# Kernel optimization log

Measured on AMD Instinct MI355X. Metric: run time of the kernel, lower is better.

Reference implementation:

```python
import jax, jax.numpy as jnp
import numpy as np

B, C, T = 128, 19, 1000

def _conv2d(x, w, pad, groups=1):
    return jax.lax.conv_general_dilated(x, w, (1, 1), [(pad[0], pad[0]), (pad[1], pad[1])],
                                        dimension_numbers=('NCHW', 'OIHW', 'NCHW'),
                                        feature_group_count=groups)

def _conv1d(x, w, pad):
    return jax.lax.conv_general_dilated(x, w, (1,), [(pad, pad)],
                                        dimension_numbers=('NCH', 'OIH', 'NCH'))

def _bn(x, g, b, axis=1):
    # eval-mode BatchNorm with running_mean=0, running_var=1 -> pure affine
    shp = [1] * x.ndim
    shp[axis] = -1
    return x * g.reshape(shp) + b.reshape(shp)

def _gat(x, W, a_src, a_dst, bias, src, dst, ew):
    # GATConv, concat=False (head mean); messages scaled by external edge weight ew
    N = x.shape[0]
    H, D = a_src.shape
    h = (x @ W).reshape(N, H, D)
    e = jax.nn.leaky_relu((h * a_src).sum(-1)[src] + (h * a_dst).sum(-1)[dst], 0.2)  # [E,H]
    emax = jax.ops.segment_max(e, dst, num_segments=N)
    ee = jnp.exp(e - emax[dst])
    alpha = ee / (jax.ops.segment_sum(ee, dst, num_segments=N)[dst] + 1e-16)
    msg = (alpha * ew[:, None])[:, :, None] * h[src]  # [E,H,D]
    return jax.ops.segment_sum(msg, dst, num_segments=N).mean(1) + bias

def setup_inputs():
    key = jax.random.key(0)
    ks = iter(jax.random.split(key, 48))
    def nrm(shape, s=0.1):
        return jax.random.normal(next(ks), shape, jnp.float32) * s
    ii = np.arange(C)
    base = np.arange(B)[:, None] * C
    src = (base + np.repeat(ii, C)[None, :]).reshape(-1)
    dst = (base + np.tile(ii, C)[None, :]).reshape(-1)
    return {
        'x': nrm((B, C, T), 1.0),
        'conv1_w': nrm((16, 1, 1, 25)),
        'bn1_g': 1.0 + nrm((16,)), 'bn1_b': nrm((16,)),
        'depth_w': nrm((16, 1, C, 1)),
        'bn2_g': 1.0 + nrm((16,)), 'bn2_b': nrm((16,)),
        'se_w1': nrm((16, 4)), 'se_w2': nrm((4, 16)),
        'sep_w': nrm((16, 16, 1, 16)),
        'bn3_g': 1.0 + nrm((16,)), 'bn3_b': nrm((16,)),
        'ms_w0': nrm((16, 1, 15)), 'ms_g0': 1.0 + nrm((16,)), 'ms_b0': nrm((16,)),
        'ms_w1': nrm((16, 1, 25)), 'ms_g1': 1.0 + nrm((16,)), 'ms_b1': nrm((16,)),
        'ms_w2': nrm((16, 1, 35)), 'ms_g2': 1.0 + nrm((16,)), 'ms_b2': nrm((16,)),
        'adj_w': nrm((32, 1)), 'adj_b': nrm((1,)),
        'gat1_w': nrm((32, 8 * 64), 0.05), 'gat1_as': nrm((8, 64)), 'gat1_ad': nrm((8, 64)), 'gat1_bias': nrm((64,)),
        'skip1_w': nrm((32, 64)), 'skip1_b': nrm((64,)),
        'bng1_g': 1.0 + nrm((64,)), 'bng1_b': nrm((64,)),
        'gat2_w': nrm((64, 8 * 64), 0.05), 'gat2_as': nrm((8, 64)), 'gat2_ad': nrm((8, 64)), 'gat2_bias': nrm((64,)),
        'bng2_g': 1.0 + nrm((64,)), 'bng2_b': nrm((64,)),
        'cls_w1': nrm((64, 64)), 'cls_b1': nrm((64,)),
        'cls_w2': nrm((64, 2)), 'cls_b2': nrm((2,)),
        'edge_index': jnp.asarray(np.stack([src, dst]), dtype=jnp.int32),
        'batch_idx': jnp.repeat(jnp.arange(B, dtype=jnp.int32), C),
    }

def reference(x, conv1_w, bn1_g, bn1_b, depth_w, bn2_g, bn2_b, se_w1, se_w2, sep_w, bn3_g, bn3_b,
              ms_w0, ms_g0, ms_b0, ms_w1, ms_g1, ms_b1, ms_w2, ms_g2, ms_b2,
              adj_w, adj_b, gat1_w, gat1_as, gat1_ad, gat1_bias, skip1_w, skip1_b, bng1_g, bng1_b,
              gat2_w, gat2_as, gat2_ad, gat2_bias, bng2_g, bng2_b, cls_w1, cls_b1, cls_w2, cls_b2,
              edge_index, batch_idx):
    Bn, Cn, Tn = x.shape
    gelu = lambda v: jax.nn.gelu(v, approximate=False)
    # --- EEGNet-style frontend ---
    y = _conv2d(x[:, None], conv1_w, (0, 12))                 # [B,16,C,T]
    y = _bn(y, bn1_g, bn1_b)
    y = _conv2d(y, depth_w, (0, 0), groups=16)                # depthwise over channels -> [B,16,1,T]
    y = jax.nn.elu(_bn(y, bn2_g, bn2_b))
    s = y.mean((2, 3))                                        # SE squeeze [B,16]
    s = jax.nn.sigmoid(gelu(s @ se_w1) @ se_w2)
    y = y * s[:, :, None, None]
    y = y.reshape(Bn, 16, 1, Tn // 4, 4).mean(-1)             # AvgPool2d((1,4))
    y = jax.nn.elu(_bn(_conv2d(y, sep_w, (0, 8)), bn3_g, bn3_b))
    yv = y.mean((2, 3))                                       # AdaptiveAvgPool2d((C,1)): 1->C replicates
    y_nodes = jnp.broadcast_to(yv[:, None, :], (Bn, Cn, 16)).reshape(Bn * Cn, 16)
    # --- per-channel multiscale conv1d ---
    z = x.reshape(Bn * Cn, 1, Tn)
    acc = jax.nn.elu(_bn(_conv1d(z, ms_w0, 7), ms_g0, ms_b0))
    acc = acc + jax.nn.elu(_bn(_conv1d(z, ms_w1, 12), ms_g1, ms_b1))
    acc = acc + jax.nn.elu(_bn(_conv1d(z, ms_w2, 17), ms_g2, ms_b2))
    z = (acc / 3.0).mean(-1)                                  # AdaptiveAvgPool1d(1) -> [N,16]
    feat = jnp.concatenate([y_nodes, z], axis=1)              # [N,32]
    # --- edge-weighted GAT stack ---
    scores = jax.nn.sigmoid(feat @ adj_w + adj_b).reshape(-1)
    src, dst = edge_index[0], edge_index[1]
    ew = scores[src] * scores[dst]
    h = _gat(feat, gat1_w, gat1_as, gat1_ad, gat1_bias, src, dst, ew)
    h = gelu(_bn(h, bng1_g, bng1_b) + feat @ skip1_w + skip1_b)
    h2 = _gat(h, gat2_w, gat2_as, gat2_ad, gat2_bias, src, dst, ew)
    h = gelu(_bn(h2, bng2_g, bng2_b) + h2)
    # --- global mean pool + classifier ---
    gs = jax.ops.segment_sum(h, batch_idx, num_segments=Bn)
    cnt = jax.ops.segment_sum(jnp.ones((Bn * Cn, 1), h.dtype), batch_idx, num_segments=Bn)
    g = gs / cnt
    return gelu(g @ cls_w1 + cls_b1) @ cls_w2 + cls_b2
```

## Files before the change

kernel.cpp:

```cpp
#include <hip/hip_runtime.h>
#include <hip/hip_bf16.h>
#include <math.h>

#define BATCH 128
#define NCH 19
#define TLEN 1000
#define NNODES (BATCH * NCH)

__device__ __forceinline__ float eluf(float x) {
  return fmaxf(x, 0.f) + (__expf(fminf(x, 0.f)) - 1.f);
}
__device__ __forceinline__ float geluf(float x) { return 0.5f * x * (1.f + erff(x * 0.70710678118654752f)); }
__device__ __forceinline__ float sigf(float x) { return 1.f / (1.f + __expf(-x)); }
__device__ __forceinline__ float lrelu(float x) { return x > 0.f ? x : 0.2f * x; }

__global__ __launch_bounds__(256) void k_pool(
    const float* __restrict__ x, const float* __restrict__ w1,
    const float* __restrict__ bn1g, const float* __restrict__ bn1b,
    const float* __restrict__ dw, const float* __restrict__ bn2g,
    const float* __restrict__ bn2b, float* __restrict__ y4g,
    float* __restrict__ ssum) {
  int blk = blockIdx.x;
  int b = blk >> 4, f = blk & 15;
  int tid = threadIdx.x;
  __shared__ float xw[1024];
  __shared__ float dws[19], w1s[25];
  __shared__ float redw[4];
  if (tid < 19) dws[tid] = dw[f * 19 + tid];
  else if (tid >= 32 && tid < 57) w1s[tid - 32] = w1[f * 25 + tid - 32];
  __syncthreads();
  const float* xb = x + (size_t)b * NCH * TLEN;
  for (int i = tid; i < 1024; i += 256) {
    int t = i - 12;
    float v = 0.f;
    if (t >= 0 && t < TLEN) {
#pragma unroll
      for (int c = 0; c < 19; c++) v += dws[c] * xb[c * TLEN + t];
    }
    xw[i] = v;
  }
  __syncthreads();
  float g1 = bn1g[f], b1 = bn1b[f];
  float g2 = bn2g[f], b2 = bn2b[f];
  float sumdw = 0.f;
#pragma unroll
  for (int c = 0; c < 19; c++) sumdw += dws[c];
  float scale = g2 * g1, cb = g2 * b1 * sumdw + b2;
  float part = 0.f;
  if (tid < 250) {
    float pool = 0.f;
#pragma unroll
    for (int q = 0; q < 4; q++) {
      int t = 4 * tid + q;
      float acc = 0.f;
#pragma unroll
      for (int k = 0; k < 25; k++) acc += w1s[k] * xw[t + k];
      pool += eluf(scale * acc + cb);
    }
    part = pool;
    y4g[(size_t)(b * 16 + f) * 250 + tid] = pool * 0.25f;
  }
  int lane = tid & 63, wid = tid >> 6;
  for (int off = 32; off > 0; off >>= 1) part += __shfl_down(part, off, 64);
  if (lane == 0) redw[wid] = part;
  __syncthreads();
  if (tid == 0) ssum[b * 16 + f] = redw[0] + redw[1] + redw[2] + redw[3];
}

__global__ __launch_bounds__(256) void k_sep(
    const float* __restrict__ y4g, const float* __restrict__ ssum,
    const float* __restrict__ sew1, const float* __restrict__ sew2,
    const float* __restrict__ sw, const float* __restrict__ g3,
    const float* __restrict__ b3, float* __restrict__ yv) {
  int blk = blockIdx.x;
  int b = blk >> 4, fo = blk & 15;
  int tid = threadIdx.x;
  __shared__ float yloc[16 * 268];
  __shared__ float sws[256];
  __shared__ float s_s[16], se_s[16], u4[4];
  __shared__ float redw[4];
  sws[tid] = sw[fo * 256 + tid];
  if (tid < 16) s_s[tid] = ssum[b * 16 + tid] * (1.f / 1000.f);
  __syncthreads();
  if (tid < 4) {
    float a = 0.f;
#pragma unroll
    for (int ff = 0; ff < 16; ff++) a += s_s[ff] * sew1[ff * 4 + tid];
    u4[tid] = geluf(a);
  }
  __syncthreads();
  if (tid < 16) {
    float a = 0.f;
#pragma unroll
    for (int j = 0; j < 4; j++) a += u4[j] * sew2[j * 16 + tid];
    se_s[tid] = sigf(a);
  }
  __syncthreads();
#pragma unroll
  for (int fi = 0; fi < 16; fi++) {
    float sc = se_s[fi];
    const float* yr = y4g + (size_t)(b * 16 + fi) * 250;
    for (int j = tid; j < 268; j += 256) {
      float v = (j >= 8 && j < 258) ? yr[j - 8] * sc : 0.f;
      yloc[fi * 268 + j] = v;
    }
  }
  __syncthreads();
  float accsum = 0.f;
  if (tid < 251) {
    float acc = 0.f;
#pragma unroll
    for (int fi = 0; fi < 16; fi++) {
      const float* yr = &yloc[fi * 268 + tid];
      const float* wp = &sws[fi * 16];
#pragma unroll
      for (int k = 0; k < 16; k++) acc += yr[k] * wp[k];
    }
    accsum = eluf(g3[fo] * acc + b3[fo]);
  }
  int lane = tid & 63, wid = tid >> 6;
  for (int off = 32; off > 0; off >>= 1)
    accsum += __shfl_down(accsum, off, 64);
  if (lane == 0) redw[wid] = accsum;
  __syncthreads();
  if (tid == 0)
    yv[b * 16 + fo] = (redw[0] + redw[1] + redw[2] + redw[3]) * (1.f / 251.f);
}

#define RP 8
__global__ __launch_bounds__(256) void k_ms(
    const float* __restrict__ x, const float* __restrict__ w0,
    const float* __restrict__ ga0, const float* __restrict__ bb0,
    const float* __restrict__ w1, const float* __restrict__ ga1,
    const float* __restrict__ bb1, const float* __restrict__ w2,
    const float* __restrict__ ga2, const float* __restrict__ bb2,
    const float* __restrict__ yv, float* __restrict__ feat) {
  int n = blockIdx.x, tid = threadIdx.x;
  __shared__ float xr[1034];
  __shared__ float wst[1200];
  __shared__ float red[256];
  for (int i = tid; i < 1034; i += 256) {
    int t = i - 17;
    xr[i] = (t >= 0 && t < TLEN) ? x[(size_t)n * TLEN + t] : 0.f;
  }
  for (int i = tid; i < 240; i += 256) wst[i] = w0[i];
  for (int i = tid; i < 400; i += 256) wst[240 + i] = w1[i];
  for (int i = tid; i < 560; i += 256) wst[640 + i] = w2[i];
  __syncthreads();

  int f = tid & 15, plane = tid >> 4;
  float z = 0.f;

  {
    float w[15];
#pragma unroll
    for (int k = 0; k < 15; k++) w[k] = wst[f * 15 + k];
    float g = ga0[f], c = bb0[f];
    for (int base = plane * RP; base < TLEN; base += 16 * RP) {
      float xv[14 + RP];
#pragma unroll
      for (int i = 0; i < 14 + RP; i++) xv[i] = xr[base + 10 + i];
#pragma unroll
      for (int r = 0; r < RP; r++) {
        float a = 0.f;
#pragma unroll
        for (int k = 0; k < 15; k++) a += xv[r + k] * w[k];
        z += eluf(g * a + c);
      }
    }
  }
  {
    float w[25];
#pragma unroll
    for (int k = 0; k < 25; k++) w[k] = wst[240 + f * 25 + k];
    float g = ga1[f], c = bb1[f];
    for (int base = plane * RP; base < TLEN; base += 16 * RP) {
      float xv[24 + RP];
#pragma unroll
      for (int i = 0; i < 24 + RP; i++) xv[i] = xr[base + 5 + i];
#pragma unroll
      for (int r = 0; r < RP; r++) {
        float a = 0.f;
#pragma unroll
        for (int k = 0; k < 25; k++) a += xv[r + k] * w[k];
        z += eluf(g * a + c);
      }
    }
  }
  {
    float w[35];
#pragma unroll
    for (int k = 0; k < 35; k++) w[k] = wst[640 + f * 35 + k];
    float g = ga2[f], c = bb2[f];
    for (int base = plane * RP; base < TLEN; base += 16 * RP) {
      float xv[34 + RP];
#pragma unroll
      for (int i = 0; i < 34 + RP; i++) xv[i] = xr[base + i];
#pragma unroll
      for (int r = 0; r < RP; r++) {
        float a = 0.f;
#pragma unroll
        for (int k = 0; k < 35; k++) a += xv[r + k] * w[k];
        z += eluf(g * a + c);
      }
    }
  }

  red[tid] = z;
  __syncthreads();
  for (int s = 128; s >= 16; s >>= 1) {
    if (tid < s) red[tid] += red[tid + s];
    __syncthreads();
  }
  if (tid < 16) {
    feat[(size_t)n * 32 + 16 + tid] = red[tid] * (1.f / 3000.f);
    feat[(size_t)n * 32 + tid] = yv[(n / 19) * 16 + tid];
  }
}

__global__ __launch_bounds__(256) void k_gat1(
    const float* __restrict__ feat, const float* __restrict__ adjw,
    const float* __restrict__ adjb, const float* __restrict__ gw,
    const float* __restrict__ gas, const float* __restrict__ gad,
    const float* __restrict__ gbias, const float* __restrict__ skw,
    const float* __restrict__ skb, const float* __restrict__ bg,
    const float* __restrict__ bb, float* __restrict__ sc_out,
    float* __restrict__ hfeat) {
  int b = blockIdx.x, tid = threadIdx.x;
  __shared__ float fb[19 * 32];
  __shared__ float h1[19 * 512];
  __shared__ float as_s[19 * 8], ad_s[19 * 8], sc_s[19];
  __shared__ float watt[19 * 8 * 19];
  for (int i = tid; i < 19 * 32; i += 256) fb[i] = feat[(size_t)b * 19 * 32 + i];
  __syncthreads();
  for (int idx = tid; idx < 19 * 512; idx += 256) {
    int i = idx >> 9, o = idx & 511;
    const float* fr = &fb[i * 32];
    float a = 0.f;
#pragma unroll
    for (int c = 0; c < 32; c++) a += fr[c] * gw[c * 512 + o];
    h1[idx] = a;
  }
  if (tid < 19) {
    float a = adjb[0];
#pragma unroll
    for (int c = 0; c < 32; c++) a += fb[tid * 32 + c] * adjw[c];
    float s = sigf(a);
    sc_s[tid] = s;
    sc_out[b * 19 + tid] = s;
  }
  __syncthreads();
  if (tid < 152) {
    int i = tid / 8, h = tid & 7;
    float a = 0.f, d2 = 0.f;
#pragma unroll
    for (int d = 0; d < 64; d++) {
      float hv = h1[i * 512 + h * 64 + d];
      a += hv * gas[h * 64 + d];
      d2 += hv * gad[h * 64 + d];
    }
    as_s[tid] = a;
    ad_s[tid] = d2;
  }
  __syncthreads();
  if (tid < 152) {
    int j = tid / 8, h = tid & 7;
    float adj_ = ad_s[j * 8 + h];
    float ev[19], m = -1e30f;
#pragma unroll
    for (int i = 0; i < 19; i++) {
      float e = lrelu(as_s[i * 8 + h] + adj_);
      ev[i] = e;
      m = fmaxf(m, e);
    }
    float den = 0.f;
#pragma unroll
    for (int i = 0; i < 19; i++) {
      ev[i] = __expf(ev[i] - m);
      den += ev[i];
    }
    float inv = 1.f / (den + 1e-16f);
    float scj = sc_s[j];
#pragma unroll
    for (int i = 0; i < 19; i++)
      watt[(j * 8 + h) * 19 + i] = ev[i] * inv * sc_s[i] * scj;
  }
  __syncthreads();
  for (int idx = tid; idx < 19 * 64; idx += 256) {
    int j = idx >> 6, d = idx & 63;
    float acc = 0.f;
#pragma unroll
    for (int h = 0; h < 8; h++) {
      const float* wr = &watt[(j * 8 + h) * 19];
      float a = 0.f;
#pragma unroll
      for (int i = 0; i < 19; i++) a += wr[i] * h1[i * 512 + h * 64 + d];
      acc += a;
    }
    float om = acc * 0.125f + gbias[d];
    float v = bg[d] * om + bb[d];
    float sk = skb[d];
    const float* fr = &fb[j * 32];
#pragma unroll
    for (int c = 0; c < 32; c++) sk += fr[c] * skw[c * 64 + d];
    hfeat[(size_t)(b * 19 + j) * 64 + d] = geluf(v + sk);
  }
}

__global__ __launch_bounds__(256) void k_gat2(
    const float* __restrict__ hfeat, const float* __restrict__ sc_ws,
    const float* __restrict__ gw, const float* __restrict__ gas,
    const float* __restrict__ gad, const float* __restrict__ gbias,
    const float* __restrict__ bg, const float* __restrict__ bb,
    const float* __restrict__ cw1, const float* __restrict__ cb1,
    const float* __restrict__ cw2, const float* __restrict__ cb2,
    float* __restrict__ out) {
  int b = blockIdx.x, tid = threadIdx.x;
  __shared__ float hb[19 * 64];
  __shared__ float h2[19 * 512];
  __shared__ float as_s[19 * 8], ad_s[19 * 8], sc_s[19];
  __shared__ float watt[19 * 8 * 19];
  __shared__ float hout[19 * 64];
  __shared__ float gpool[64], u_s[64];
  for (int i = tid; i < 19 * 64; i += 256) hb[i] = hfeat[(size_t)b * 19 * 64 + i];
  if (tid < 19) sc_s[tid] = sc_ws[b * 19 + tid];
  __syncthreads();
  for (int idx = tid; idx < 19 * 512; idx += 256) {
    int i = idx >> 9, o = idx & 511;
    const float* hr = &hb[i * 64];
    float a = 0.f;
#pragma unroll
    for (int c = 0; c < 64; c++) a += hr[c] * gw[c * 512 + o];
    h2[idx] = a;
  }
  __syncthreads();
  if (tid < 152) {
    int i = tid / 8, h = tid & 7;
    float a = 0.f, d2 = 0.f;
#pragma unroll
    for (int d = 0; d < 64; d++) {
      float hv = h2[i * 512 + h * 64 + d];
      a += hv * gas[h * 64 + d];
      d2 += hv * gad[h * 64 + d];
    }
    as_s[tid] = a;
    ad_s[tid] = d2;
  }
  __syncthreads();
  if (tid < 152) {
    int j = tid / 8, h = tid & 7;
    float adj_ = ad_s[j * 8 + h];
    float ev[19], m = -1e30f;
#pragma unroll
    for (int i = 0; i < 19; i++) {
      float e = lrelu(as_s[i * 8 + h] + adj_);
      ev[i] = e;
      m = fmaxf(m, e);
    }
    float den = 0.f;
#pragma unroll
    for (int i = 0; i < 19; i++) {
      ev[i] = __expf(ev[i] - m);
      den += ev[i];
    }
    float inv = 1.f / (den + 1e-16f);
    float scj = sc_s[j];
#pragma unroll
    for (int i = 0; i < 19; i++)
      watt[(j * 8 + h) * 19 + i] = ev[i] * inv * sc_s[i] * scj;
  }
  __syncthreads();
  for (int idx = tid; idx < 19 * 64; idx += 256) {
    int j = idx >> 6, d = idx & 63;
    float acc = 0.f;
#pragma unroll
    for (int h = 0; h < 8; h++) {
      const float* wr = &watt[(j * 8 + h) * 19];
      float a = 0.f;
#pragma unroll
      for (int i = 0; i < 19; i++) a += wr[i] * h2[i * 512 + h * 64 + d];
      acc += a;
    }
    float om = acc * 0.125f + gbias[d];
    float v = bg[d] * om + bb[d] + om;
    hout[idx] = geluf(v);
  }
  __syncthreads();
  if (tid < 64) {
    float a = 0.f;
#pragma unroll
    for (int j = 0; j < 19; j++) a += hout[j * 64 + tid];
    gpool[tid] = a * (1.f / 19.f);
  }
  __syncthreads();
  if (tid < 64) {
    float a = cb1[tid];
#pragma unroll
    for (int d = 0; d < 64; d++) a += gpool[d] * cw1[d * 64 + tid];
    u_s[tid] = geluf(a);
  }
  __syncthreads();
  if (tid < 2) {
    float a = cb2[tid];
#pragma unroll
    for (int e = 0; e < 64; e++) a += u_s[e] * cw2[e * 2 + tid];
    out[b * 2 + tid] = a;
  }
}

extern "C" void kernel_launch(void* const* d_in, const int* in_sizes, int n_in,
                              void* d_out, int out_size, void* d_ws,
                              size_t ws_size, hipStream_t stream) {
  (void)in_sizes; (void)n_in; (void)out_size; (void)ws_size;
  const float* x = (const float*)d_in[0];
  const float* conv1_w = (const float*)d_in[1];
  const float* bn1_g = (const float*)d_in[2];
  const float* bn1_b = (const float*)d_in[3];
  const float* depth_w = (const float*)d_in[4];
  const float* bn2_g = (const float*)d_in[5];
  const float* bn2_b = (const float*)d_in[6];
  const float* se_w1 = (const float*)d_in[7];
  const float* se_w2 = (const float*)d_in[8];
  const float* sep_w = (const float*)d_in[9];
  const float* bn3_g = (const float*)d_in[10];
  const float* bn3_b = (const float*)d_in[11];
  const float* ms_w0 = (const float*)d_in[12];
  const float* ms_g0 = (const float*)d_in[13];
  const float* ms_b0 = (const float*)d_in[14];
  const float* ms_w1 = (const float*)d_in[15];
  const float* ms_g1 = (const float*)d_in[16];
  const float* ms_b1 = (const float*)d_in[17];
  const float* ms_w2 = (const float*)d_in[18];
  const float* ms_g2 = (const float*)d_in[19];
  const float* ms_b2 = (const float*)d_in[20];
  const float* adj_w = (const float*)d_in[21];
  const float* adj_b = (const float*)d_in[22];
  const float* gat1_w = (const float*)d_in[23];
  const float* gat1_as = (const float*)d_in[24];
  const float* gat1_ad = (const float*)d_in[25];
  const float* gat1_bias = (const float*)d_in[26];
  const float* skip1_w = (const float*)d_in[27];
  const float* skip1_b = (const float*)d_in[28];
  const float* bng1_g = (const float*)d_in[29];
  const float* bng1_b = (const float*)d_in[30];
  const float* gat2_w = (const float*)d_in[31];
  const float* gat2_as = (const float*)d_in[32];
  const float* gat2_ad = (const float*)d_in[33];
  const float* gat2_bias = (const float*)d_in[34];
  const float* bng2_g = (const float*)d_in[35];
  const float* bng2_b = (const float*)d_in[36];
  const float* cls_w1 = (const float*)d_in[37];
  const float* cls_b1 = (const float*)d_in[38];
  const float* cls_w2 = (const float*)d_in[39];
  const float* cls_b2 = (const float*)d_in[40];

  float* ws = (float*)d_ws;
  float* yv = ws;
  float* feat = ws + 2048;
  float* scw = ws + 79872;
  float* hfeat = ws + 82304;
  float* y4g = ws + 237952;
  float* ssum = ws + 749952;

  hipLaunchKernelGGL(k_pool, dim3(BATCH * 16), dim3(256), 0, stream,
                     x, conv1_w, bn1_g, bn1_b, depth_w, bn2_g, bn2_b, y4g, ssum);
  hipLaunchKernelGGL(k_sep, dim3(BATCH * 16), dim3(256), 0, stream,
                     y4g, ssum, se_w1, se_w2, sep_w, bn3_g, bn3_b, yv);
  hipLaunchKernelGGL(k_ms, dim3(NNODES), dim3(256), 0, stream,
                     x, ms_w0, ms_g0, ms_b0, ms_w1, ms_g1, ms_b1, ms_w2,
                     ms_g2, ms_b2, yv, feat);
  hipLaunchKernelGGL(k_gat1, dim3(BATCH), dim3(256), 0, stream,
                     feat, adj_w, adj_b, gat1_w, gat1_as, gat1_ad, gat1_bias,
                     skip1_w, skip1_b, bng1_g, bng1_b, scw, hfeat);
  hipLaunchKernelGGL(k_gat2, dim3(BATCH), dim3(256), 0, stream,
                     hfeat, scw, gat2_w, gat2_as, gat2_ad, gat2_bias, bng2_g,
                     bng2_b, cls_w1, cls_b1, cls_w2, cls_b2, (float*)d_out);
}
```

Measured before the change: 378.2 us.

## Fuse temporal conv, SE, separable conv and both GAT layers into one kernel

Replaces the pool, sep, gat1 and gat2 kernels with a single per-batch kernel that keeps the depthwise/temporal conv outputs, SE gating, separable conv, and both GAT layers in shared memory. This removes intermediate global-memory buffers and three kernel launches. The trade-off is much lower parallelism for the conv stages: the work formerly spread over 2048 blocks now runs in 128 blocks, with a less unrolled separable-conv loop.

```diff
diff --git a/kernel.cpp b/kernel.cpp
--- a/kernel.cpp
+++ b/kernel.cpp
@@ -13,119 +13,6 @@
 __device__ __forceinline__ float geluf(float x) { return 0.5f * x * (1.f + erff(x * 0.70710678118654752f)); }
 __device__ __forceinline__ float sigf(float x) { return 1.f / (1.f + __expf(-x)); }
 __device__ __forceinline__ float lrelu(float x) { return x > 0.f ? x : 0.2f * x; }
-
-__global__ __launch_bounds__(256) void k_pool(
-    const float* __restrict__ x, const float* __restrict__ w1,
-    const float* __restrict__ bn1g, const float* __restrict__ bn1b,
-    const float* __restrict__ dw, const float* __restrict__ bn2g,
-    const float* __restrict__ bn2b, float* __restrict__ y4g,
-    float* __restrict__ ssum) {
-  int blk = blockIdx.x;
-  int b = blk >> 4, f = blk & 15;
-  int tid = threadIdx.x;
-  __shared__ float xw[1024];
-  __shared__ float dws[19], w1s[25];
-  __shared__ float redw[4];
-  if (tid < 19) dws[tid] = dw[f * 19 + tid];
-  else if (tid >= 32 && tid < 57) w1s[tid - 32] = w1[f * 25 + tid - 32];
-  __syncthreads();
-  const float* xb = x + (size_t)b * NCH * TLEN;
-  for (int i = tid; i < 1024; i += 256) {
-    int t = i - 12;
-    float v = 0.f;
-    if (t >= 0 && t < TLEN) {
-#pragma unroll
-      for (int c = 0; c < 19; c++) v += dws[c] * xb[c * TLEN + t];
-    }
-    xw[i] = v;
-  }
-  __syncthreads();
-  float g1 = bn1g[f], b1 = bn1b[f];
-  float g2 = bn2g[f], b2 = bn2b[f];
-  float sumdw = 0.f;
-#pragma unroll
-  for (int c = 0; c < 19; c++) sumdw += dws[c];
-  float scale = g2 * g1, cb = g2 * b1 * sumdw + b2;
-  float part = 0.f;
-  if (tid < 250) {
-    float pool = 0.f;
-#pragma unroll
-    for (int q = 0; q < 4; q++) {
-      int t = 4 * tid + q;
-      float acc = 0.f;
-#pragma unroll
-      for (int k = 0; k < 25; k++) acc += w1s[k] * xw[t + k];
-      pool += eluf(scale * acc + cb);
-    }
-    part = pool;
-    y4g[(size_t)(b * 16 + f) * 250 + tid] = pool * 0.25f;
-  }
-  int lane = tid & 63, wid = tid >> 6;
-  for (int off = 32; off > 0; off >>= 1) part += __shfl_down(part, off, 64);
-  if (lane == 0) redw[wid] = part;
-  __syncthreads();
-  if (tid == 0) ssum[b * 16 + f] = redw[0] + redw[1] + redw[2] + redw[3];
-}
-
-__global__ __launch_bounds__(256) void k_sep(
-    const float* __restrict__ y4g, const float* __restrict__ ssum,
-    const float* __restrict__ sew1, const float* __restrict__ sew2,
-    const float* __restrict__ sw, const float* __restrict__ g3,
-    const float* __restrict__ b3, float* __restrict__ yv) {
-  int blk = blockIdx.x;
-  int b = blk >> 4, fo = blk & 15;
-  int tid = threadIdx.x;
-  __shared__ float yloc[16 * 268];
-  __shared__ float sws[256];
-  __shared__ float s_s[16], se_s[16], u4[4];
-  __shared__ float redw[4];
-  sws[tid] = sw[fo * 256 + tid];
-  if (tid < 16) s_s[tid] = ssum[b * 16 + tid] * (1.f / 1000.f);
-  __syncthreads();
-  if (tid < 4) {
-    float a = 0.f;
-#pragma unroll
-    for (int ff = 0; ff < 16; ff++) a += s_s[ff] * sew1[ff * 4 + tid];
-    u4[tid] = geluf(a);
-  }
-  __syncthreads();
-  if (tid < 16) {
-    float a = 0.f;
-#pragma unroll
-    for (int j = 0; j < 4; j++) a += u4[j] * sew2[j * 16 + tid];
-    se_s[tid] = sigf(a);
-  }
-  __syncthreads();
-#pragma unroll
-  for (int fi = 0; fi < 16; fi++) {
-    float sc = se_s[fi];
-    const float* yr = y4g + (size_t)(b * 16 + fi) * 250;
-    for (int j = tid; j < 268; j += 256) {
-      float v = (j >= 8 && j < 258) ? yr[j - 8] * sc : 0.f;
-      yloc[fi * 268 + j] = v;
-    }
-  }
-  __syncthreads();
-  float accsum = 0.f;
-  if (tid < 251) {
-    float acc = 0.f;
-#pragma unroll
-    for (int fi = 0; fi < 16; fi++) {
-      const float* yr = &yloc[fi * 268 + tid];
-      const float* wp = &sws[fi * 16];
-#pragma unroll
-      for (int k = 0; k < 16; k++) acc += yr[k] * wp[k];
-    }
-    accsum = eluf(g3[fo] * acc + b3[fo]);
-  }
-  int lane = tid & 63, wid = tid >> 6;
-  for (int off = 32; off > 0; off >>= 1)
-    accsum += __shfl_down(accsum, off, 64);
-  if (lane == 0) redw[wid] = accsum;
-  __syncthreads();
-  if (tid == 0)
-    yv[b * 16 + fo] = (redw[0] + redw[1] + redw[2] + redw[3]) * (1.f / 251.f);
-}
 
 #define RP 8
 __global__ __launch_bounds__(256) void k_ms(
@@ -134,7 +21,7 @@
     const float* __restrict__ w1, const float* __restrict__ ga1,
     const float* __restrict__ bb1, const float* __restrict__ w2,
     const float* __restrict__ ga2, const float* __restrict__ bb2,
-    const float* __restrict__ yv, float* __restrict__ feat) {
+    float* __restrict__ feat) {
   int n = blockIdx.x, tid = threadIdx.x;
   __shared__ float xr[1034];
   __shared__ float wst[1200];
@@ -212,64 +99,211 @@
     if (tid < s) red[tid] += red[tid + s];
     __syncthreads();
   }
+  if (tid < 16) feat[(size_t)n * 32 + 16 + tid] = red[tid] * (1.f / 3000.f);
+}
+
+#define OF_XW 0
+#define OF_Y4 8200
+#define OF_DWS 12232
+#define OF_W1S 12536
+#define OF_SS 12936
+#define OF_SE 12952
+#define OF_U4 12968
+#define OF_RED 12992
+#define OF_SWS 0
+#define OF_FB 0
+#define OF_H 608
+#define OF_WATT 10336
+#define OF_AS 13224
+#define OF_AD 13376
+#define OF_SC 13528
+#define OF_HB 13548
+#define OF_HOUT 14764
+#define OF_GP 15980
+#define OF_US 16044
+#define OF_YV 16320
+
+__global__ __launch_bounds__(256) void k_fused(
+    const float* __restrict__ x, const float* __restrict__ w1,
+    const float* __restrict__ bn1g, const float* __restrict__ bn1b,
+    const float* __restrict__ dw, const float* __restrict__ bn2g,
+    const float* __restrict__ bn2b, const float* __restrict__ sew1,
+    const float* __restrict__ sew2, const float* __restrict__ sw,
+    const float* __restrict__ g3, const float* __restrict__ b3,
+    const float* __restrict__ adjw, const float* __restrict__ adjb,
+    const float* __restrict__ g1w, const float* __restrict__ g1as,
+    const float* __restrict__ g1ad, const float* __restrict__ g1bias,
+    const float* __restrict__ skw, const float* __restrict__ skb,
+    const float* __restrict__ bg1, const float* __restrict__ bb1g,
+    const float* __restrict__ g2w, const float* __restrict__ g2as,
+    const float* __restrict__ g2ad, const float* __restrict__ g2bias,
+    const float* __restrict__ bg2, const float* __restrict__ bb2g,
+    const float* __restrict__ cw1, const float* __restrict__ cb1,
+    const float* __restrict__ cw2, const float* __restrict__ cb2,
+    const float* __restrict__ feat, float* __restrict__ out) {
+  __shared__ float S[16336];
+  int b = blockIdx.x, tid = threadIdx.x;
+  int lane = tid & 63, wid = tid >> 6;
+
+  for (int i = tid; i < 304; i += 256) S[OF_DWS + i] = dw[i];
+  for (int i = tid; i < 400; i += 256) S[OF_W1S + i] = w1[i];
+  __syncthreads();
+
+  const float* xb = x + (size_t)b * NCH * TLEN;
+  for (int half = 0; half < 2; half++) {
+    for (int i = tid; i < 1024; i += 256) {
+      int t = i - 12;
+      float xv[19];
+      if (t >= 0 && t < TLEN) {
+#pragma unroll
+        for (int c = 0; c < 19; c++) xv[c] = xb[c * TLEN + t];
+      } else {
+#pragma unroll
+        for (int c = 0; c < 19; c++) xv[c] = 0.f;
+      }
+#pragma unroll
+      for (int fo = 0; fo < 8; fo++) {
+        const float* dr = &S[OF_DWS + (half * 8 + fo) * 19];
+        float a = 0.f;
+#pragma unroll
+        for (int c = 0; c < 19; c++) a += dr[c] * xv[c];
+        S[OF_XW + fo * 1025 + i] = a;
+      }
+    }
+    __syncthreads();
+    float pools[8];
+#pragma unroll
+    for (int fo = 0; fo < 8; fo++) pools[fo] = 0.f;
+    if (tid < 250) {
+#pragma unroll
+      for (int fo = 0; fo < 8; fo++) {
+        int f = half * 8 + fo;
+        float scale = bn2g[f] * bn1g[f];
+        float sumdw = 0.f;
+#pragma unroll
+        for (int c = 0; c < 19; c++) sumdw += S[OF_DWS + f * 19 + c];
+        float cb = bn2g[f] * bn1b[f] * sumdw + bn2b[f];
+        const float* wr = &S[OF_W1S + f * 25];
+        float win[28];
+#pragma unroll
+        for (int i2 = 0; i2 < 28; i2++)
+          win[i2] = S[OF_XW + fo * 1025 + 4 * tid + i2];
+        float pool = 0.f;
+#pragma unroll
+        for (int q = 0; q < 4; q++) {
+          float acc = 0.f;
+#pragma unroll
+          for (int k = 0; k < 25; k++) acc += wr[k] * win[q + k];
+          pool += eluf(scale * acc + cb);
+        }
+        pools[fo] = pool;
+        S[OF_Y4 + f * 252 + tid] = pool * 0.25f;
+      }
+    }
+#pragma unroll
+    for (int fo = 0; fo < 8; fo++) {
+      float v = pools[fo];
+      for (int off = 32; off > 0; off >>= 1) v += __shfl_down(v, off, 64);
+      if (lane == 0) S[OF_RED + wid * 8 + fo] = v;
+    }
+    __syncthreads();
+    if (tid < 8)
+      S[OF_SS + half * 8 + tid] =
+          (S[OF_RED + tid] + S[OF_RED + 8 + tid] + S[OF_RED + 16 + tid] +
+           S[OF_RED + 24 + tid]) * (1.f / 1000.f);
+    __syncthreads();
+  }
+  if (tid < 4) {
+    float a = 0.f;
+#pragma unroll
+    for (int ff = 0; ff < 16; ff++) a += S[OF_SS + ff] * sew1[ff * 4 + tid];
+    S[OF_U4 + tid] = geluf(a);
+  }
+  __syncthreads();
   if (tid < 16) {
-    feat[(size_t)n * 32 + 16 + tid] = red[tid] * (1.f / 3000.f);
-    feat[(size_t)n * 32 + tid] = yv[(n / 19) * 16 + tid];
-  }
-}
-
-__global__ __launch_bounds__(256) void k_gat1(
-    const float* __restrict__ feat, const float* __restrict__ adjw,
-    const float* __restrict__ adjb, const float* __restrict__ gw,
-    const float* __restrict__ gas, const float* __restrict__ gad,
-    const float* __restrict__ gbias, const float* __restrict__ skw,
-    const float* __restrict__ skb, const float* __restrict__ bg,
-    const float* __restrict__ bb, float* __restrict__ sc_out,
-    float* __restrict__ hfeat) {
-  int b = blockIdx.x, tid = threadIdx.x;
-  __shared__ float fb[19 * 32];
-  __shared__ float h1[19 * 512];
-  __shared__ float as_s[19 * 8], ad_s[19 * 8], sc_s[19];
-  __shared__ float watt[19 * 8 * 19];
-  for (int i = tid; i < 19 * 32; i += 256) fb[i] = feat[(size_t)b * 19 * 32 + i];
+    float a = 0.f;
+#pragma unroll
+    for (int j = 0; j < 4; j++) a += S[OF_U4 + j] * sew2[j * 16 + tid];
+    S[OF_SE + tid] = sigf(a);
+  }
+  __syncthreads();
+  for (int idx = tid; idx < 4000; idx += 256) {
+    int f = idx / 250, p = idx - f * 250;
+    S[OF_Y4 + f * 252 + p] *= S[OF_SE + f];
+  }
+  for (int i = tid; i < 4096; i += 256) S[OF_SWS + i] = sw[i];
+  __syncthreads();
+  {
+    int fo = tid >> 4, l16 = tid & 15;
+    float g3v = g3[fo], b3v = b3[fo];
+    float accsum = 0.f;
+    for (int o = l16; o < 251; o += 16) {
+      float acc = 0.f;
+      int klo = (o < 8) ? (8 - o) : 0;
+      int khi = (258 - o < 16) ? (258 - o) : 16;
+      for (int fi = 0; fi < 16; fi++) {
+        const float* yr = &S[OF_Y4 + fi * 252 + o - 8];
+        const float* wp = &S[OF_SWS + fo * 256 + fi * 16];
+        for (int k = klo; k < khi; k++) acc += yr[k] * wp[k];
+      }
+      accsum += eluf(g3v * acc + b3v);
+    }
+    accsum += __shfl_down(accsum, 8, 16);
+    accsum += __shfl_down(accsum, 4, 16);
+    accsum += __shfl_down(accsum, 2, 16);
+    accsum += __shfl_down(accsum, 1, 16);
+    if (l16 == 0) S[OF_YV + fo] = accsum * (1.f / 251.f);
+  }
+  __syncthreads();
+
+  float* fb = &S[OF_FB];
+  float* h = &S[OF_H];
+  float* watt = &S[OF_WATT];
+  float* as_s = &S[OF_AS];
+  float* ad_s = &S[OF_AD];
+  float* sc_s = &S[OF_SC];
+  float* hb = &S[OF_HB];
+  float* hout = &S[OF_HOUT];
+  for (int idx = tid; idx < 19 * 32; idx += 256) {
+    int i = idx >> 5, c = idx & 31;
+    fb[idx] = (c < 16) ? S[OF_YV + c] : feat[(size_t)(b * 19 + i) * 32 + c];
+  }
   __syncthreads();
   for (int idx = tid; idx < 19 * 512; idx += 256) {
     int i = idx >> 9, o = idx & 511;
     const float* fr = &fb[i * 32];
     float a = 0.f;
 #pragma unroll
-    for (int c = 0; c < 32; c++) a += fr[c] * gw[c * 512 + o];
-    h1[idx] = a;
+    for (int c = 0; c < 32; c++) a += fr[c] * g1w[c * 512 + o];
+    h[idx] = a;
   }
   if (tid < 19) {
     float a = adjb[0];
 #pragma unroll
     for (int c = 0; c < 32; c++) a += fb[tid * 32 + c] * adjw[c];
-    float s = sigf(a);
-    sc_s[tid] = s;
-    sc_out[b * 19 + tid] = s;
+    sc_s[tid] = sigf(a);
   }
   __syncthreads();
   if (tid < 152) {
-    int i = tid / 8, h = tid & 7;
+    int i = tid / 8, hh = tid & 7;
     float a = 0.f, d2 = 0.f;
 #pragma unroll
     for (int d = 0; d < 64; d++) {
-      float hv = h1[i * 512 + h * 64 + d];
-      a += hv * gas[h * 64 + d];
-      d2 += hv * gad[h * 64 + d];
+      float hv = h[i * 512 + hh * 64 + d];
+      a += hv * g1as[hh * 64 + d];
+      d2 += hv * g1ad[hh * 64 + d];
     }
     as_s[tid] = a;
     ad_s[tid] = d2;
   }
   __syncthreads();
   if (tid < 152) {
-    int j = tid / 8, h = tid & 7;
-    float adj_ = ad_s[j * 8 + h];
+    int j = tid / 8, hh = tid & 7;
+    float adj_ = ad_s[j * 8 + hh];
     float ev[19], m = -1e30f;
 #pragma unroll
     for (int i = 0; i < 19; i++) {
-      float e = lrelu(as_s[i * 8 + h] + adj_);
+      float e = lrelu(as_s[i * 8 + hh] + adj_);
       ev[i] = e;
       m = fmaxf(m, e);
     }
@@ -283,77 +317,59 @@
     float scj = sc_s[j];
 #pragma unroll
     for (int i = 0; i < 19; i++)
-      watt[(j * 8 + h) * 19 + i] = ev[i] * inv * sc_s[i] * scj;
+      watt[(j * 8 + hh) * 19 + i] = ev[i] * inv * sc_s[i] * scj;
   }
   __syncthreads();
   for (int idx = tid; idx < 19 * 64; idx += 256) {
     int j = idx >> 6, d = idx & 63;
     float acc = 0.f;
 #pragma unroll
-    for (int h = 0; h < 8; h++) {
-      const float* wr = &watt[(j * 8 + h) * 19];
+    for (int hh = 0; hh < 8; hh++) {
+      const float* wr = &watt[(j * 8 + hh) * 19];
       float a = 0.f;
 #pragma unroll
-      for (int i = 0; i < 19; i++) a += wr[i] * h1[i * 512 + h * 64 + d];
+      for (int i = 0; i < 19; i++) a += wr[i] * h[i * 512 + hh * 64 + d];
       acc += a;
     }
-    float om = acc * 0.125f + gbias[d];
-    float v = bg[d] * om + bb[d];
+    float om = acc * 0.125f + g1bias[d];
+    float v = bg1[d] * om + bb1g[d];
     float sk = skb[d];
     const float* fr = &fb[j * 32];
 #pragma unroll
     for (int c = 0; c < 32; c++) sk += fr[c] * skw[c * 64 + d];
-    hfeat[(size_t)(b * 19 + j) * 64 + d] = geluf(v + sk);
-  }
-}
-
-__global__ __launch_bounds__(256) void k_gat2(
-    const float* __restrict__ hfeat, const float* __restrict__ sc_ws,
-    const float* __restrict__ gw, const float* __restrict__ gas,
-    const float* __restrict__ gad, const float* __restrict__ gbias,
-    const float* __restrict__ bg, const float* __restrict__ bb,
-    const float* __restrict__ cw1, const float* __restrict__ cb1,
-    const float* __restrict__ cw2, const float* __restrict__ cb2,
-    float* __restrict__ out) {
-  int b = blockIdx.x, tid = threadIdx.x;
-  __shared__ float hb[19 * 64];
-  __shared__ float h2[19 * 512];
-  __shared__ float as_s[19 * 8], ad_s[19 * 8], sc_s[19];
-  __shared__ float watt[19 * 8 * 19];
-  __shared__ float hout[19 * 64];
-  __shared__ float gpool[64], u_s[64];
-  for (int i = tid; i < 19 * 64; i += 256) hb[i] = hfeat[(size_t)b * 19 * 64 + i];
-  if (tid < 19) sc_s[tid] = sc_ws[b * 19 + tid];
-  __syncthreads();
+    hb[idx] = geluf(v + sk);
+  }
+  __syncthreads();
+
   for (int idx = tid; idx < 19 * 512; idx += 256) {
     int i = idx >> 9, o = idx & 511;
     const float* hr = &hb[i * 64];
     float a = 0.f;
 #pragma unroll
-    for (int c = 0; c < 64; c++) a += hr[c] * gw[c * 512 + o];
-    h2[idx] = a;
+    for (int c = 0; c < 64; c++) a += hr[c] * g2w[c * 512 + o];
+    h[idx] = a;
   }
   __syncthreads();
   if (tid < 152) {
-    int i = tid / 8, h = tid & 7;
+    int i = tid / 8, hh = tid & 7;
     float a = 0.f, d2 = 0.f;
 #pragma unroll
     for (int d = 0; d < 64; d++) {
-      float hv = h2[i * 512 + h * 64 + d];
-      a += hv * gas[h * 64 + d];
-      d2 += hv * gad[h * 64 + d];
+      float hv = h[i * 512 + hh * 64 + d];
+      a += hv * g2as[hh * 64 + d];
+      d2 += hv * g2ad[hh * 64 + d];
     }
     as_s[tid] = a;
     ad_s[tid] = d2;
   }
   __syncthreads();
   if (tid < 152) {
-    int j = tid / 8, h = tid & 7;
-    float adj_ = ad_s[j * 8 + h];
+    int j = tid / 8, hh = tid & 7;
+    float adj_ = ad_s[j * 8 + hh];
     float ev[19], m = -1e30f;
 #pragma unroll
     for (int i = 0; i < 19; i++) {
-      float e = lrelu(as_s[i * 8 + h] + adj_);
+      float e = lrelu(as_s[i * 8 + hh] + adj_);
       ev[i] = e;
       m = fmaxf(m, e);
     }
@@ -367,22 +383,22 @@
     float scj = sc_s[j];
 #pragma unroll
     for (int i = 0; i < 19; i++)
-      watt[(j * 8 + h) * 19 + i] = ev[i] * inv * sc_s[i] * scj;
+      watt[(j * 8 + hh) * 19 + i] = ev[i] * inv * sc_s[i] * scj;
   }
   __syncthreads();
   for (int idx = tid; idx < 19 * 64; idx += 256) {
     int j = idx >> 6, d = idx & 63;
     float acc = 0.f;
 #pragma unroll
-    for (int h = 0; h < 8; h++) {
-      const float* wr = &watt[(j * 8 + h) * 19];
+    for (int hh = 0; hh < 8; hh++) {
+      const float* wr = &watt[(j * 8 + hh) * 19];
       float a = 0.f;
 #pragma unroll
-      for (int i = 0; i < 19; i++) a += wr[i] * h2[i * 512 + h * 64 + d];
+      for (int i = 0; i < 19; i++) a += wr[i] * h[i * 512 + hh * 64 + d];
       acc += a;
     }
-    float om = acc * 0.125f + gbias[d];
-    float v = bg[d] * om + bb[d] + om;
+    float om = acc * 0.125f + g2bias[d];
+    float v = bg2[d] * om + bb2g[d] + om;
     hout[idx] = geluf(v);
   }
   __syncthreads();
@@ -390,20 +406,20 @@
     float a = 0.f;
 #pragma unroll
     for (int j = 0; j < 19; j++) a += hout[j * 64 + tid];
-    gpool[tid] = a * (1.f / 19.f);
+    S[OF_GP + tid] = a * (1.f / 19.f);
   }
   __syncthreads();
   if (tid < 64) {
     float a = cb1[tid];
 #pragma unroll
-    for (int d = 0; d < 64; d++) a += gpool[d] * cw1[d * 64 + tid];
-    u_s[tid] = geluf(a);
+    for (int d = 0; d < 64; d++) a += S[OF_GP + d] * cw1[d * 64 + tid];
+    S[OF_US + tid] = geluf(a);
   }
   __syncthreads();
   if (tid < 2) {
     float a = cb2[tid];
 #pragma unroll
-    for (int e = 0; e < 64; e++) a += u_s[e] * cw2[e * 2 + tid];
+    for (int e = 0; e < 64; e++) a += S[OF_US + e] * cw2[e * 2 + tid];
     out[b * 2 + tid] = a;
   }
 }
@@ -454,25 +470,16 @@
   const float* cls_w2 = (const float*)d_in[39];
   const float* cls_b2 = (const float*)d_in[40];
 
-  float* ws = (float*)d_ws;
-  float* yv = ws;
-  float* feat = ws + 2048;
-  float* scw = ws + 79872;
-  float* hfeat = ws + 82304;
-  float* y4g = ws + 237952;
-  float* ssum = ws + 749952;
-
-  hipLaunchKernelGGL(k_pool, dim3(BATCH * 16), dim3(256), 0, stream,
-                     x, conv1_w, bn1_g, bn1_b, depth_w, bn2_g, bn2_b, y4g, ssum);
-  hipLaunchKernelGGL(k_sep, dim3(BATCH * 16), dim3(256), 0, stream,
-                     y4g, ssum, se_w1, se_w2, sep_w, bn3_g, bn3_b, yv);
+  float* feat = (float*)d_ws;
+
   hipLaunchKernelGGL(k_ms, dim3(NNODES), dim3(256), 0, stream,
                      x, ms_w0, ms_g0, ms_b0, ms_w1, ms_g1, ms_b1, ms_w2,
-                     ms_g2, ms_b2, yv, feat);
-  hipLaunchKernelGGL(k_gat1, dim3(BATCH), dim3(256), 0, stream,
-                     feat, adj_w, adj_b, gat1_w, gat1_as, gat1_ad, gat1_bias,
-                     skip1_w, skip1_b, bng1_g, bng1_b, scw, hfeat);
-  hipLaunchKernelGGL(k_gat2, dim3(BATCH), dim3(256), 0, stream,
-                     hfeat, scw, gat2_w, gat2_as, gat2_ad, gat2_bias, bng2_g,
-                     bng2_b, cls_w1, cls_b1, cls_w2, cls_b2, (float*)d_out);
+                     ms_g2, ms_b2, feat);
+  hipLaunchKernelGGL(k_fused, dim3(BATCH), dim3(256), 0, stream,
+                     x, conv1_w, bn1_g, bn1_b, depth_w, bn2_g, bn2_b,
+                     se_w1, se_w2, sep_w, bn3_g, bn3_b,
+                     adj_w, adj_b, gat1_w, gat1_as, gat1_ad, gat1_bias,
+                     skip1_w, skip1_b, bng1_g, bng1_b,
+                     gat2_w, gat2_as, gat2_ad, gat2_bias, bng2_g, bng2_b,
+                     cls_w1, cls_b1, cls_w2, cls_b2, feat, (float*)d_out);
 }
```

Result: slower. 532.8 us (+40.9%).
